# Performance work log

Measured on AMD Instinct MI355X. Metric: run time of the kernel, lower is better.

The kernel has to match this reference:

```python
import jax, jax.numpy as jnp
import numpy as np

HID = 256      # cfg.MODEL.YOSO.HIDDEN_DIM
NPROP = 100    # cfg.MODEL.YOSO.NUM_PROPOSALS
K1 = 3         # CONV_KERNEL_SIZE_1D
K2 = 1         # CONV_KERNEL_SIZE_2D
NCLS = 80      # NUM_CLASSES
NHEAD = 8

def layernorm(x, g, b, eps=1e-5):
    m = jnp.mean(x, -1, keepdims=True)
    v = jnp.var(x, -1, keepdims=True)
    return (x - m) * jax.lax.rsqrt(v + eps) * g + b

def dysep(query, value, Wl, bl, ng, nb):
    # dynamic depthwise conv (kernel K1 along feature axis, one kernel per proposal)
    # followed by dynamic pointwise NxN conv, per torch F.conv1d semantics (cross-correlation, 'same' pad)
    w = query @ Wl + bl                      # [B,N,N+K1]
    dw = w[..., :K1]                         # [B,N,K1] depthwise kernels
    pw = w[..., K1:]                         # [B,N,N]  pointwise mixing
    C = value.shape[-1]
    pad = K1 // 2
    vp = jnp.pad(value, ((0, 0), (0, 0), (pad, pad)))
    depth = sum(dw[..., k:k + 1] * vp[..., k:k + C] for k in range(K1))
    depth = jax.nn.relu(depth)
    point = jnp.einsum('bmn,bnc->bmc', pw, depth)
    return layernorm(point, ng, nb)

def mha(x, in_w, in_b, out_w, out_b):
    B, N, E = x.shape
    d = E // NHEAD
    qkv = x @ in_w + in_b
    q, k, v = jnp.split(qkv, 3, axis=-1)
    q = q.reshape(B, N, NHEAD, d)
    k = k.reshape(B, N, NHEAD, d)
    v = v.reshape(B, N, NHEAD, d)
    att = jnp.einsum('bqhd,bkhd->bhqk', q, k) / jnp.sqrt(jnp.asarray(d, x.dtype))
    att = jax.nn.softmax(att, axis=-1)
    o = jnp.einsum('bhqk,bkhd->bqhd', att, v).reshape(B, N, E)
    return o @ out_w + out_b

def setup_inputs() -> dict:
    key = jax.random.key(0)
    ks = iter(jax.random.split(key, 64))
    B, H, W = 8, 128, 128
    E = HID * K2 * K2
    nrm = lambda *s: jax.random.normal(next(ks), s, jnp.float32) * 0.02
    bias_value = -np.log((1 - 0.01) / 0.01)
    return dict(
        features=jax.random.normal(next(ks), (B, HID, H, W), jnp.float32),
        proposal_kernels=jax.random.normal(next(ks), (B, NPROP, E), jnp.float32),
        mask_preds=jax.random.normal(next(ks), (B, NPROP, H, W), jnp.float32),
        fW=nrm(E, NPROP + K1), fb=jnp.zeros(NPROP + K1), fng=jnp.ones(E), fnb=jnp.zeros(E),
        f_norm_g=jnp.ones(E), f_norm_b=jnp.zeros(E),
        kW=nrm(E, NPROP + K1), kb=jnp.zeros(NPROP + K1), kng=jnp.ones(E), knb=jnp.zeros(E),
        k_norm_g=jnp.ones(E), k_norm_b=jnp.zeros(E),
        attn_in_w=nrm(E, 3 * E), attn_in_b=jnp.zeros(3 * E),
        attn_out_w=nrm(E, E), attn_out_b=jnp.zeros(E),
        s_norm_g=jnp.ones(E), s_norm_b=jnp.zeros(E),
        ffn_w1=nrm(HID, 2048), ffn_b1=jnp.zeros(2048),
        ffn_w2=nrm(2048, HID), ffn_b2=jnp.zeros(HID),
        ffn_norm_g=jnp.ones(HID), ffn_norm_b=jnp.zeros(HID),
        cls_w=nrm(HID, HID), cls_ln_g=jnp.ones(HID), cls_ln_b=jnp.zeros(HID),
        fc_cls_w=nrm(HID, NCLS + 1), fc_cls_b=jnp.full((NCLS + 1,), bias_value, jnp.float32),
        mask_w=nrm(3, HID, HID), mask_ln_g=jnp.ones((3, HID)), mask_ln_b=jnp.zeros((3, HID)),
        fc_mask_w=nrm(HID, HID), fc_mask_b=jnp.zeros(HID),
        train_flag=1,
    )

def reference(features, proposal_kernels, mask_preds, fW, fb, fng, fnb, f_norm_g, f_norm_b,
              kW, kb, kng, knb, k_norm_g, k_norm_b,
              attn_in_w, attn_in_b, attn_out_w, attn_out_b, s_norm_g, s_norm_b,
              ffn_w1, ffn_b1, ffn_w2, ffn_b2, ffn_norm_g, ffn_norm_b,
              cls_w, cls_ln_g, cls_ln_b, fc_cls_w, fc_cls_b,
              mask_w, mask_ln_g, mask_ln_b, fc_mask_w, fc_mask_b, train_flag):
    B, C, H, W = features.shape
    hard = (jax.nn.sigmoid(mask_preds) > 0.5).astype(features.dtype)   # hard masks (no grad path)
    f = jnp.einsum('bnhw,bchw->bnc', hard, features)                   # mask-pooled features [B,N,E]
    k = proposal_kernels.reshape(B, NPROP, -1)
    f = layernorm(f + dysep(k, f, fW, fb, fng, fnb), f_norm_g, f_norm_b)
    kk = layernorm(f + dysep(k, f, kW, kb, kng, knb), k_norm_g, k_norm_b)
    kk = layernorm(kk + mha(kk, attn_in_w, attn_in_b, attn_out_w, attn_out_b), s_norm_g, s_norm_b)
    obj = jnp.transpose(kk.reshape(B, NPROP, HID, -1), (0, 1, 3, 2))   # [B,N,K2*K2,HID]
    h = jax.nn.relu(obj @ ffn_w1 + ffn_b1)
    obj = layernorm(obj + (h @ ffn_w2 + ffn_b2), ffn_norm_g, ffn_norm_b)
    cls_feat = obj.sum(-2)                                             # [B,N,HID]
    mask_feat = obj
    if train_flag:
        cls_feat = jax.nn.relu(layernorm(cls_feat @ cls_w, cls_ln_g, cls_ln_b))
        cls_score = (cls_feat @ fc_cls_w + fc_cls_b).reshape(B, NPROP, -1)
    else:
        cls_score = None
    for i in range(mask_w.shape[0]):
        mask_feat = jax.nn.relu(layernorm(mask_feat @ mask_w[i], mask_ln_g[i], mask_ln_b[i]))
    mask_kernels = (mask_feat @ fc_mask_w + fc_mask_b)[:, :, 0, :]     # squeeze(2), K2*K2==1
    new_mask_preds = jnp.einsum('bqc,bchw->bqhw', mask_kernels, features)
    obj_out = jnp.transpose(obj, (0, 1, 3, 2)).reshape(B, NPROP, HID, K2, K2)
    return (cls_score, new_mask_preds, obj_out)
```

## Files before the change

kernel.cpp:

```cpp
#include <hip/hip_runtime.h>

typedef float f32x4 __attribute__((ext_vector_type(4)));
typedef short bfrag __attribute__((ext_vector_type(8)));
typedef short sh4 __attribute__((ext_vector_type(4)));

__device__ __forceinline__ unsigned short f2bf(float x) {
  unsigned int u = __float_as_uint(x);
  return (unsigned short)((u + 0x7FFFu + ((u >> 16) & 1u)) >> 16);
}
__device__ __forceinline__ float bf2f(unsigned short u) {
  return __uint_as_float(((unsigned int)u) << 16);
}
__device__ __forceinline__ float wred_sum(float v) {
#pragma unroll
  for (int o = 32; o > 0; o >>= 1) v += __shfl_xor(v, o);
  return v;
}
__device__ __forceinline__ float wred_max(float v) {
#pragma unroll
  for (int o = 32; o > 0; o >>= 1) v = fmaxf(v, __shfl_xor(v, o));
  return v;
}

struct Prep6 {
  const float* s[6];
  int K[6];
  int N[6];
  int base[6];
  int doff[6];
};

__global__ __launch_bounds__(256) void prep_w(Prep6 p, unsigned short* wt) {
  int t = blockIdx.x;
  int wi = 0;
#pragma unroll
  for (int i = 0; i < 5; ++i)
    if (t >= p.base[i + 1]) wi = i + 1;
  int lt = t - p.base[wi];
  int K = p.K[wi], N = p.N[wi];
  int tkn = (K + 31) >> 5;
  int tk = lt % tkn, tn = lt / tkn;
  __shared__ float tile[32][33];
  const float* src = p.s[wi];
#pragma unroll
  for (int i = 0; i < 4; ++i) {
    int flat = i * 256 + threadIdx.x;
    int kl = flat >> 5, nl = flat & 31;
    int k = tk * 32 + kl, n = tn * 32 + nl;
    tile[kl][nl] = (k < K && n < N) ? src[(size_t)k * N + n] : 0.f;
  }
  __syncthreads();
  unsigned short* dst = wt + p.doff[wi];
#pragma unroll
  for (int i = 0; i < 4; ++i) {
    int flat = i * 256 + threadIdx.x;
    int nl = flat >> 5, kl = flat & 31;
    int k = tk * 32 + kl, n = tn * 32 + nl;
    if (k < K && n < N) {
      int np = (wi < 2) ? ((n >= 3) ? n - 3 : n + 100) : n;
      dst[(size_t)np * K + k] = f2bf(tile[kl][nl]);
    }
  }
}

__global__ __launch_bounds__(256) void prep_bias(const float* __restrict__ fb_,
                                                 const float* __restrict__ kb_,
                                                 float* __restrict__ bf,
                                                 float* __restrict__ bk) {
  int t = threadIdx.x;
  if (t < 103) {
    int np = (t >= 3) ? t - 3 : t + 100;
    bf[np] = fb_[t];
    bk[np] = kb_[t];
  }
  if (t == 103) { bf[103] = 0.f; bk[103] = 0.f; }
}

struct Cast4 {
  const float* s[4];
  int n[4];
  int base[4];
  int doff[4];
};

__global__ __launch_bounds__(256) void cast_w(Cast4 cc, unsigned short* dst) {
  int t = blockIdx.x;
  int wi = 0;
#pragma unroll
  for (int i = 0; i < 3; ++i)
    if (t >= cc.base[i + 1]) wi = i + 1;
  int lt = t - cc.base[wi];
  int idx = lt * 1024 + threadIdx.x * 4;
  if (idx + 3 < cc.n[wi]) {
    float4 v = *(const float4*)(cc.s[wi] + idx);
    sh4 o;
    o[0] = (short)f2bf(v.x); o[1] = (short)f2bf(v.y);
    o[2] = (short)f2bf(v.z); o[3] = (short)f2bf(v.w);
    *(sh4*)(dst + cc.doff[wi] + idx) = o;
  }
}

__global__ __launch_bounds__(256) void pack_bits(const float* __restrict__ mask,
                                                 unsigned int* __restrict__ bits) {
  int tid = threadIdx.x;
  size_t f = (size_t)blockIdx.x * 256 + tid;
  float4 m = *(const float4*)(mask + f * 4);
  unsigned int n = (m.x > 0.f ? 1u : 0u) | (m.y > 0.f ? 2u : 0u) |
                   (m.z > 0.f ? 4u : 0u) | (m.w > 0.f ? 8u : 0u);
  n <<= ((tid & 7) * 4);
  n |= (unsigned int)__shfl_xor((int)n, 1);
  n |= (unsigned int)__shfl_xor((int)n, 2);
  n |= (unsigned int)__shfl_xor((int)n, 4);
  if ((tid & 7) == 0) bits[((size_t)blockIdx.x * 32) + (tid >> 3)] = n;
}

template <int ABF, int OBF>
__global__ __launch_bounds__(256) void gemm_mf(const void* Av,
                                               const unsigned short* __restrict__ Wt,
                                               const float* __restrict__ bias,
                                               void* Cv, int M, int K, int N, int ldc, int relu) {
  __shared__ short Al[64 * 72];
  __shared__ short Wl[64 * 72];
  int tid = threadIdx.x;
  int r0 = blockIdx.x * 64;
  int c0 = blockIdx.y * 64;
  int w = tid >> 6, lane = tid & 63, quad = lane >> 4, l15 = lane & 15;

  f32x4 acc[4];
#pragma unroll
  for (int mt = 0; mt < 4; ++mt) {
    acc[mt][0] = 0.f; acc[mt][1] = 0.f; acc[mt][2] = 0.f; acc[mt][3] = 0.f;
  }

  for (int k0 = 0; k0 < K; k0 += 64) {
    if (ABF) {
      const unsigned short* A = (const unsigned short*)Av;
#pragma unroll
      for (int p = 0; p < 2; ++p) {
        int flat = p * 256 + tid;
        int row = flat >> 3, k8 = flat & 7;
        bfrag v;
        if (r0 + row < M)
          v = *(const bfrag*)(A + (size_t)(r0 + row) * K + k0 + k8 * 8);
        else
          v = (bfrag)(short)0;
        *(bfrag*)(Al + row * 72 + k8 * 8) = v;
      }
    } else {
      const float* A = (const float*)Av;
#pragma unroll
      for (int p = 0; p < 4; ++p) {
        int flat = p * 256 + tid;
        int row = flat >> 4, c4 = flat & 15;
        sh4 o4;
        if (r0 + row < M) {
          float4 v = *(const float4*)(A + (size_t)(r0 + row) * K + k0 + c4 * 4);
          o4[0] = (short)f2bf(v.x); o4[1] = (short)f2bf(v.y);
          o4[2] = (short)f2bf(v.z); o4[3] = (short)f2bf(v.w);
        } else {
          o4[0] = 0; o4[1] = 0; o4[2] = 0; o4[3] = 0;
        }
        *(sh4*)(Al + row * 72 + c4 * 4) = o4;
      }
    }
#pragma unroll
    for (int p = 0; p < 2; ++p) {
      int flat = p * 256 + tid;
      int row = flat >> 3, k8 = flat & 7;
      bfrag v;
      if (c0 + row < N)
        v = *(const bfrag*)(Wt + (size_t)(c0 + row) * K + k0 + k8 * 8);
      else
        v = (bfrag)(short)0;
      *(bfrag*)(Wl + row * 72 + k8 * 8) = v;
    }
    __syncthreads();
#pragma unroll
    for (int kk = 0; kk < 2; ++kk) {
      bfrag bv = *(const bfrag*)(Wl + (w * 16 + l15) * 72 + kk * 32 + quad * 8);
#pragma unroll
      for (int mt = 0; mt < 4; ++mt) {
        bfrag av = *(const bfrag*)(Al + (mt * 16 + l15) * 72 + kk * 32 + quad * 8);
        acc[mt] = __builtin_amdgcn_mfma_f32_16x16x32_bf16(av, bv, acc[mt], 0, 0, 0);
      }
    }
    __syncthreads();
  }
  int col = c0 + w * 16 + l15;
  if (col < N) {
    float bv = bias ? bias[col] : 0.f;
#pragma unroll
    for (int mt = 0; mt < 4; ++mt)
#pragma unroll
      for (int r = 0; r < 4; ++r) {
        int m = r0 + mt * 16 + quad * 4 + r;
        if (m < M) {
          float v = acc[mt][r] + bv;
          if (relu) v = fmaxf(v, 0.f);
          if (OBF)
            ((unsigned short*)Cv)[(size_t)m * ldc + col] = f2bf(v);
          else
            ((float*)Cv)[(size_t)m * ldc + col] = v;
        }
      }
  }
}

__global__ __launch_bounds__(512, 4) void phaseA(const unsigned int* __restrict__ bits,
                                                 const float* __restrict__ feat,
                                                 float* __restrict__ partial) {
  int tid = threadIdx.x;
  int ks = blockIdx.x;
  int ct = blockIdx.y;
  int b  = blockIdx.z;
  __shared__ short Al[2][112 * 72];
  __shared__ short Bl[2][128 * 72];
  int w = tid >> 6, lane = tid & 63, quad = lane >> 4, l15 = lane & 15;

  int rbase = tid >> 4;
  int c4 = tid & 15;
  const float* frow = feat + (size_t)(b * 256 + ct * 128 + rbase) * 16384 + c4 * 4;

  int arow = tid >> 2, q = tid & 3;
  bool aact = tid < 400;
  const unsigned int* brow = bits + (size_t)(b * 100 + arow) * 512 + (q >> 1);

  f32x4 acc[7];
#pragma unroll
  for (int mt = 0; mt < 7; ++mt) {
    acc[mt][0] = 0.f; acc[mt][1] = 0.f; acc[mt][2] = 0.f; acc[mt][3] = 0.f;
  }

  for (int z = tid; z < 384; z += 512) {
    int bufi = z / 192, rem = z % 192;
    sh4 zz; zz[0] = 0; zz[1] = 0; zz[2] = 0; zz[3] = 0;
    *(sh4*)(&Al[bufi][(100 + (rem >> 4)) * 72 + (rem & 15) * 4]) = zz;
  }

  int k0 = ks * 512;
  {
    float4 bpf[4];
    unsigned int awd = 0;
#pragma unroll
    for (int p = 0; p < 4; ++p)
      bpf[p] = *(const float4*)(frow + (size_t)p * 32 * 16384 + k0);
    if (aact) awd = brow[k0 >> 5];
#pragma unroll
    for (int p = 0; p < 4; ++p) {
      int row = rbase + 32 * p;
      sh4 o4b;
      o4b[0] = (short)f2bf(bpf[p].x);
      o4b[1] = (short)f2bf(bpf[p].y);
      o4b[2] = (short)f2bf(bpf[p].z);
      o4b[3] = (short)f2bf(bpf[p].w);
      *(sh4*)(&Bl[0][row * 72 + c4 * 4]) = o4b;
    }
    if (aact) {
      unsigned int hw16 = (awd >> ((q & 1) * 16)) & 0xFFFFu;
      bfrag e0, e1;
#pragma unroll
      for (int i = 0; i < 8; ++i) e0[i] = ((hw16 >> i) & 1u) ? (short)0x3F80 : (short)0;
#pragma unroll
      for (int i = 0; i < 8; ++i) e1[i] = ((hw16 >> (i + 8)) & 1u) ? (short)0x3F80 : (short)0;
      *(bfrag*)(&Al[0][arow * 72 + q * 16]) = e0;
      *(bfrag*)(&Al[0][arow * 72 + q * 16 + 8]) = e1;
    }
  }
  __syncthreads();

  int cur = 0;
  for (int st = 0; st < 8; ++st) {
    float4 bpf[4];
    unsigned int awd = 0;
    if (st < 7) {
      int kb = k0 + (st + 1) * 64;
#pragma unroll
      for (int p = 0; p < 4; ++p)
        bpf[p] = *(const float4*)(frow + (size_t)p * 32 * 16384 + kb);
      if (aact) awd = brow[kb >> 5];
    }
#pragma unroll
    for (int kk = 0; kk < 2; ++kk) {
      bfrag bv = *(const bfrag*)(&Bl[cur][(w * 16 + l15) * 72 + kk * 32 + quad * 8]);
#pragma unroll
      for (int mt = 0; mt < 7; ++mt) {
        bfrag av = *(const bfrag*)(&Al[cur][(mt * 16 + l15) * 72 + kk * 32 + quad * 8]);
        acc[mt] = __builtin_amdgcn_mfma_f32_16x16x32_bf16(av, bv, acc[mt], 0, 0, 0);
      }
    }
    __builtin_amdgcn_sched_barrier(0);
    if (st < 7) {
      int nxt = cur ^ 1;
#pragma unroll
      for (int p = 0; p < 4; ++p) {
        int row = rbase + 32 * p;
        sh4 o4b;
        o4b[0] = (short)f2bf(bpf[p].x);
        o4b[1] = (short)f2bf(bpf[p].y);
        o4b[2] = (short)f2bf(bpf[p].z);
        o4b[3] = (short)f2bf(bpf[p].w);
        *(sh4*)(&Bl[nxt][row * 72 + c4 * 4]) = o4b;
      }
      if (aact) {
        unsigned int hw16 = (awd >> ((q & 1) * 16)) & 0xFFFFu;
        bfrag e0, e1;
#pragma unroll
        for (int i = 0; i < 8; ++i) e0[i] = ((hw16 >> i) & 1u) ? (short)0x3F80 : (short)0;
#pragma unroll
        for (int i = 0; i < 8; ++i) e1[i] = ((hw16 >> (i + 8)) & 1u) ? (short)0x3F80 : (short)0;
        *(bfrag*)(&Al[nxt][arow * 72 + q * 16]) = e0;
        *(bfrag*)(&Al[nxt][arow * 72 + q * 16 + 8]) = e1;
      }
    }
    __syncthreads();
    cur ^= 1;
  }

  float* pb = partial + (size_t)(b * 32 + ks) * (100 * 256) + ct * 128 + w * 16 + l15;
#pragma unroll
  for (int mt = 0; mt < 7; ++mt)
#pragma unroll
    for (int r = 0; r < 4; ++r) {
      int m = mt * 16 + quad * 4 + r;
      if (m < 100) pb[(size_t)m * 256] = acc[mt][r];
    }
}

__global__ __launch_bounds__(256) void reduceA(const float* __restrict__ partial,
                                               float* __restrict__ fm) {
  int gid = blockIdx.x * 256 + threadIdx.x;
  int c = gid & 255, row = gid >> 8;
  int b = row / 100, n = row % 100;
  float s = 0.f;
#pragma unroll
  for (int ks = 0; ks < 32; ++ks)
    s += partial[((size_t)(b * 32 + ks) * 100 + n) * 256 + c];
  fm[(size_t)row * 256 + c] = s;
}

__global__ __launch_bounds__(256) void pointdw(const float* __restrict__ fm,
                                               const float* __restrict__ wbuf,
                                               float* __restrict__ point) {
  int tid = threadIdx.x;
  int b = blockIdx.y, c0 = blockIdx.x * 32;
  __shared__ float dl[100 * 33];
  for (int flat = tid; flat < 3200; flat += 256) {
    int n = flat >> 5, cl = flat & 31, c = c0 + cl;
    const float* fr = fm + (size_t)(b * 100 + n) * 256;
    const float* wr = wbuf + (size_t)(b * 100 + n) * 104;
    float x0 = (c > 0) ? fr[c - 1] : 0.f;
    float x1 = fr[c];
    float x2 = (c < 255) ? fr[c + 1] : 0.f;
    float d = wr[100] * x0 + wr[101] * x1 + wr[102] * x2;
    dl[n * 33 + cl] = fmaxf(d, 0.f);
  }
  __syncthreads();
  int cl = tid & 31, mg = tid >> 5;
  for (int m = mg; m < 100; m += 8) {
    const float4* pw4 = (const float4*)(wbuf + (size_t)(b * 100 + m) * 104);
    float a = 0.f;
#pragma unroll
    for (int n4 = 0; n4 < 25; ++n4) {
      float4 wv = pw4[n4];
      a += wv.x * dl[(n4 * 4 + 0) * 33 + cl] + wv.y * dl[(n4 * 4 + 1) * 33 + cl]
         + wv.z * dl[(n4 * 4 + 2) * 33 + cl] + wv.w * dl[(n4 * 4 + 3) * 33 + cl];
    }
    point[(size_t)(b * 100 + m) * 256 + c0 + cl] = a;
  }
}

__global__ __launch_bounds__(256) void ln2_kernel(const float* __restrict__ x,
                                                  const float* __restrict__ resid,
                                                  const float* __restrict__ g1, const float* __restrict__ b1,
                                                  const float* __restrict__ g2, const float* __restrict__ b2,
                                                  float* __restrict__ out) {
  int tid = threadIdx.x;
  int row = blockIdx.x * 4 + (tid >> 6);
  int lane = tid & 63;
  size_t base = (size_t)row * 256 + lane * 4;
  float4 v = *(const float4*)(x + base);
  float mean = wred_sum(v.x + v.y + v.z + v.w) * (1.f / 256.f);
  float d0 = v.x - mean, d1 = v.y - mean, d2 = v.z - mean, d3 = v.w - mean;
  float rs = rsqrtf(wred_sum(d0 * d0 + d1 * d1 + d2 * d2 + d3 * d3) * (1.f / 256.f) + 1e-5f);
  float4 gv = *(const float4*)(g1 + lane * 4);
  float4 bv = *(const float4*)(b1 + lane * 4);
  float4 rv = *(const float4*)(resid + base);
  float y0 = rv.x + d0 * rs * gv.x + bv.x;
  float y1 = rv.y + d1 * rs * gv.y + bv.y;
  float y2 = rv.z + d2 * rs * gv.z + bv.z;
  float y3 = rv.w + d3 * rs * gv.w + bv.w;
  float mean2 = wred_sum(y0 + y1 + y2 + y3) * (1.f / 256.f);
  float e0 = y0 - mean2, e1 = y1 - mean2, e2 = y2 - mean2, e3 = y3 - mean2;
  float rs2 = rsqrtf(wred_sum(e0 * e0 + e1 * e1 + e2 * e2 + e3 * e3) * (1.f / 256.f) + 1e-5f);
  float4 g2v = *(const float4*)(g2 + lane * 4);
  float4 b2v = *(const float4*)(b2 + lane * 4);
  float4 o;
  o.x = e0 * rs2 * g2v.x + b2v.x;
  o.y = e1 * rs2 * g2v.y + b2v.y;
  o.z = e2 * rs2 * g2v.z + b2v.z;
  o.w = e3 * rs2 * g2v.w + b2v.w;
  *(float4*)(out + base) = o;
}

__global__ __launch_bounds__(256) void ln_kernel(const float* __restrict__ x,
                                                 const float* __restrict__ res,
                                                 const float* __restrict__ g, const float* __restrict__ bb,
                                                 float* __restrict__ out, int relu,
                                                 float* __restrict__ copy2) {
  int tid = threadIdx.x;
  int row = blockIdx.x * 4 + (tid >> 6);
  int lane = tid & 63;
  size_t base = (size_t)row * 256 + lane * 4;
  float4 v = *(const float4*)(x + base);
  if (res) {
    float4 rv = *(const float4*)(res + base);
    v.x += rv.x; v.y += rv.y; v.z += rv.z; v.w += rv.w;
  }
  float mean = wred_sum(v.x + v.y + v.z + v.w) * (1.f / 256.f);
  float d0 = v.x - mean, d1 = v.y - mean, d2 = v.z - mean, d3 = v.w - mean;
  float rs = rsqrtf(wred_sum(d0 * d0 + d1 * d1 + d2 * d2 + d3 * d3) * (1.f / 256.f) + 1e-5f);
  float4 gv = *(const float4*)(g + lane * 4);
  float4 bv = *(const float4*)(bb + lane * 4);
  float4 o;
  o.x = d0 * rs * gv.x + bv.x;
  o.y = d1 * rs * gv.y + bv.y;
  o.z = d2 * rs * gv.z + bv.z;
  o.w = d3 * rs * gv.w + bv.w;
  if (relu) {
    o.x = fmaxf(o.x, 0.f); o.y = fmaxf(o.y, 0.f);
    o.z = fmaxf(o.z, 0.f); o.w = fmaxf(o.w, 0.f);
  }
  *(float4*)(out + base) = o;
  if (copy2) *(float4*)(copy2 + base) = o;
}

__global__ __launch_bounds__(256) void attn_kernel(const float* __restrict__ qkv,
                                                   float* __restrict__ obuf) {
  int tid = threadIdx.x;
  int b = blockIdx.y, h = blockIdx.x;
  __shared__ float ktj[100 * 32];
  __shared__ unsigned short vl[100 * 32];
  __shared__ float sl[100 * 100];
  const float* base = qkv + (size_t)b * 100 * 768;
  for (int flat = tid; flat < 3200; flat += 256) {
    int j = flat >> 5, dd = flat & 31;
    ktj[j * 32 + dd] = base[(size_t)j * 768 + 256 + h * 32 + dd];
    vl[j * 32 + dd] = f2bf(base[(size_t)j * 768 + 512 + h * 32 + dd]);
  }
  __syncthreads();
  {
    int i = tid >> 1;
    int jh = (tid & 1) * 50;
    int qi = (i < 100) ? i : 0;
    const float4* q4 = (const float4*)(base + (size_t)qi * 768 + h * 32);
    float4 q[8];
#pragma unroll
    for (int d4 = 0; d4 < 8; ++d4) q[d4] = q4[d4];
    if (i < 100) {
      for (int jj = 0; jj < 50; ++jj) {
        int j = jh + jj;
        const float4* kr = (const float4*)(ktj + j * 32);
        float a = 0.f;
#pragma unroll
        for (int d4 = 0; d4 < 8; ++d4) {
          float4 kv = kr[d4];
          a += q[d4].x * kv.x + q[d4].y * kv.y + q[d4].z * kv.z + q[d4].w * kv.w;
        }
        sl[i * 100 + j] = a * 0.17677669529663687f;
      }
    }
  }
  __syncthreads();
  int w = tid >> 6, lane = tid & 63;
  for (int r = w; r < 100; r += 4) {
    float x0 = sl[r * 100 + lane];
    float x1 = (lane + 64 < 100) ? sl[r * 100 + lane + 64] : -1e30f;
    float mx = wred_max(fmaxf(x0, x1));
    float e0 = __expf(x0 - mx);
    float e1 = (lane + 64 < 100) ? __expf(x1 - mx) : 0.f;
    float inv = 1.f / wred_sum(e0 + e1);
    sl[r * 100 + lane] = e0 * inv;
    if (lane + 64 < 100) sl[r * 100 + lane + 64] = e1 * inv;
  }
  __syncthreads();
  for (int flat = tid; flat < 3200; flat += 256) {
    int i = flat >> 5, dd = flat & 31;
    float a = 0.f;
#pragma unroll 4
    for (int j = 0; j < 100; ++j) a += sl[i * 100 + j] * bf2f(vl[j * 32 + dd]);
    obuf[(size_t)(b * 100 + i) * 256 + h * 32 + dd] = a;
  }
}

__global__ __launch_bounds__(256) void head_fused(
    const float* __restrict__ objb,
    const unsigned short* __restrict__ whd,
    const float* __restrict__ cls_g, const float* __restrict__ cls_b,
    const float* __restrict__ fcclsb,
    const float* __restrict__ mask_g, const float* __restrict__ mask_b,
    const float* __restrict__ fcmb,
    float* __restrict__ out_cls, unsigned short* __restrict__ mk16) {
  const int WH_CLS = 0, WH_FCCLS = 65536, WH_M = 86272, WH_FCM = 282880;
  int tid = threadIdx.x, wv = tid >> 6, lane = tid & 63;
  int row = blockIdx.x;
  __shared__ float xs[256];
  __shared__ float x0s[256];
  __shared__ float ps[4][256];
  if (wv == 0) {
    float4 v = *(const float4*)(objb + (size_t)row * 256 + lane * 4);
    *(float4*)(&xs[lane * 4]) = v;
    *(float4*)(&x0s[lane * 4]) = v;
  }
  __syncthreads();
  int c = lane * 4;
  int kb = wv * 64;

  for (int li = 0; li < 3; ++li) {
    const unsigned short* W = whd + WH_M + li * 65536;
    float a0 = 0.f, a1 = 0.f, a2 = 0.f, a3 = 0.f;
#pragma unroll 8
    for (int k = kb; k < kb + 64; ++k) {
      float xk = xs[k];
      sh4 w4 = *(const sh4*)(W + (size_t)k * 256 + c);
      a0 += xk * bf2f((unsigned short)w4[0]);
      a1 += xk * bf2f((unsigned short)w4[1]);
      a2 += xk * bf2f((unsigned short)w4[2]);
      a3 += xk * bf2f((unsigned short)w4[3]);
    }
    ps[wv][c] = a0; ps[wv][c + 1] = a1; ps[wv][c + 2] = a2; ps[wv][c + 3] = a3;
    __syncthreads();
    float s0 = ps[0][c] + ps[1][c] + ps[2][c] + ps[3][c];
    float s1 = ps[0][c + 1] + ps[1][c + 1] + ps[2][c + 1] + ps[3][c + 1];
    float s2 = ps[0][c + 2] + ps[1][c + 2] + ps[2][c + 2] + ps[3][c + 2];
    float s3 = ps[0][c + 3] + ps[1][c + 3] + ps[2][c + 3] + ps[3][c + 3];
    float mean = wred_sum(s0 + s1 + s2 + s3) * (1.f / 256.f);
    float d0 = s0 - mean, d1 = s1 - mean, d2 = s2 - mean, d3 = s3 - mean;
    float rs = rsqrtf(wred_sum(d0 * d0 + d1 * d1 + d2 * d2 + d3 * d3) * (1.f / 256.f) + 1e-5f);
    float4 gv = *(const float4*)(mask_g + li * 256 + c);
    float4 bv = *(const float4*)(mask_b + li * 256 + c);
    float4 o;
    o.x = fmaxf(d0 * rs * gv.x + bv.x, 0.f);
    o.y = fmaxf(d1 * rs * gv.y + bv.y, 0.f);
    o.z = fmaxf(d2 * rs * gv.z + bv.z, 0.f);
    o.w = fmaxf(d3 * rs * gv.w + bv.w, 0.f);
    __syncthreads();
    *(float4*)(&xs[c]) = o;
    __syncthreads();
  }
  {
    const unsigned short* W = whd + WH_FCM;
    float a0 = 0.f, a1 = 0.f, a2 = 0.f, a3 = 0.f;
#pragma unroll 8
    for (int k = kb; k < kb + 64; ++k) {
      float xk = xs[k];
      sh4 w4 = *(const sh4*)(W + (size_t)k * 256 + c);
      a0 += xk * bf2f((unsigned short)w4[0]);
      a1 += xk * bf2f((unsigned short)w4[1]);
      a2 += xk * bf2f((unsigned short)w4[2]);
      a3 += xk * bf2f((unsigned short)w4[3]);
    }
    ps[wv][c] = a0; ps[wv][c + 1] = a1; ps[wv][c + 2] = a2; ps[wv][c + 3] = a3;
    __syncthreads();
    if (wv == 0) {
      float s0 = ps[0][c] + ps[1][c] + ps[2][c] + ps[3][c];
      float s1 = ps[0][c + 1] + ps[1][c + 1] + ps[2][c + 1] + ps[3][c + 1];
      float s2 = ps[0][c + 2] + ps[1][c + 2] + ps[2][c + 2] + ps[3][c + 2];
      float s3 = ps[0][c + 3] + ps[1][c + 3] + ps[2][c + 3] + ps[3][c + 3];
      float4 bv = *(const float4*)(fcmb + c);
      sh4 o;
      o[0] = (short)f2bf(s0 + bv.x); o[1] = (short)f2bf(s1 + bv.y);
      o[2] = (short)f2bf(s2 + bv.z); o[3] = (short)f2bf(s3 + bv.w);
      *(sh4*)(mk16 + (size_t)row * 256 + c) = o;
    }
    __syncthreads();
  }
  {
    const unsigned short* W = whd + WH_CLS;
    float a0 = 0.f, a1 = 0.f, a2 = 0.f, a3 = 0.f;
#pragma unroll 8
    for (int k = kb; k < kb + 64; ++k) {
      float xk = x0s[k];
      sh4 w4 = *(const sh4*)(W + (size_t)k * 256 + c);
      a0 += xk * bf2f((unsigned short)w4[0]);
      a1 += xk * bf2f((unsigned short)w4[1]);
      a2 += xk * bf2f((unsigned short)w4[2]);
      a3 += xk * bf2f((unsigned short)w4[3]);
    }
    ps[wv][c] = a0; ps[wv][c + 1] = a1; ps[wv][c + 2] = a2; ps[wv][c + 3] = a3;
    __syncthreads();
    float s0 = ps[0][c] + ps[1][c] + ps[2][c] + ps[3][c];
    float s1 = ps[0][c + 1] + ps[1][c + 1] + ps[2][c + 1] + ps[3][c + 1];
    float s2 = ps[0][c + 2] + ps[1][c + 2] + ps[2][c + 2] + ps[3][c + 2];
    float s3 = ps[0][c + 3] + ps[1][c + 3] + ps[2][c + 3] + ps[3][c + 3];
    float mean = wred_sum(s0 + s1 + s2 + s3) * (1.f / 256.f);
    float d0 = s0 - mean, d1 = s1 - mean, d2 = s2 - mean, d3 = s3 - mean;
    float rs = rsqrtf(wred_sum(d0 * d0 + d1 * d1 + d2 * d2 + d3 * d3) * (1.f / 256.f) + 1e-5f);
    float4 gv = *(const float4*)(cls_g + c);
    float4 bv = *(const float4*)(cls_b + c);
    float4 o;
    o.x = fmaxf(d0 * rs * gv.x + bv.x, 0.f);
    o.y = fmaxf(d1 * rs * gv.y + bv.y, 0.f);
    o.z = fmaxf(d2 * rs * gv.z + bv.z, 0.f);
    o.w = fmaxf(d3 * rs * gv.w + bv.w, 0.f);
    __syncthreads();
    *(float4*)(&xs[c]) = o;
    __syncthreads();
  }
  {
    const unsigned short* W = whd + WH_FCCLS;
    float a0 = 0.f, a1 = 0.f;
#pragma unroll 8
    for (int k = kb; k < kb + 64; ++k) {
      float xk = xs[k];
      a0 += xk * bf2f(W[(size_t)k * 81 + lane]);
      if (lane < 17) a1 += xk * bf2f(W[(size_t)k * 81 + 64 + lane]);
    }
    ps[wv][lane] = a0;
    if (lane < 17) ps[wv][64 + lane] = a1;
    __syncthreads();
    if (wv == 0) {
      float s = ps[0][lane] + ps[1][lane] + ps[2][lane] + ps[3][lane];
      out_cls[(size_t)row * 81 + lane] = s + fcclsb[lane];
      if (lane < 17) {
        float s2 = ps[0][64 + lane] + ps[1][64 + lane] + ps[2][64 + lane] + ps[3][64 + lane];
        out_cls[(size_t)row * 81 + 64 + lane] = s2 + fcclsb[64 + lane];
      }
    }
  }
}

__global__ __launch_bounds__(256, 4) void phaseE(const unsigned short* __restrict__ mk16,
                                                 const float* __restrict__ feat,
                                                 float* __restrict__ out) {
  int tid = threadIdx.x;
  int b = blockIdx.y;
  int hw0 = blockIdx.x * 128;
  int w = tid >> 6, lane = tid & 63, quad = lane >> 4, l15 = lane & 15;
  f32x4 acc[7][2];
#pragma unroll
  for (int mt = 0; mt < 7; ++mt)
#pragma unroll
    for (int nt = 0; nt < 2; ++nt) {
      acc[mt][nt][0] = 0.f; acc[mt][nt][1] = 0.f; acc[mt][nt][2] = 0.f; acc[mt][nt][3] = 0.f;
    }
  size_t fb = (size_t)b * 256 * 16384;
  int hwl = hw0 + w * 32 + l15;
  const unsigned short* mkb_b = mk16 + (size_t)b * 100 * 256;
  for (int kk = 0; kk < 8; ++kk) {
    bfrag bv[2];
#pragma unroll
    for (int nt = 0; nt < 2; ++nt) {
#pragma unroll
      for (int j = 0; j < 8; ++j) {
        float v = feat[fb + (size_t)(kk * 32 + quad * 8 + j) * 16384 + hwl + nt * 16];
        bv[nt][j] = (short)f2bf(v);
      }
    }
    bfrag av[7];
#pragma unroll
    for (int mt = 0; mt < 7; ++mt) {
      int row = mt * 16 + l15;
      int rr = (row < 100) ? row : 0;
      av[mt] = *(const bfrag*)(mkb_b + (size_t)rr * 256 + kk * 32 + quad * 8);
    }
#pragma unroll
    for (int mt = 0; mt < 7; ++mt) {
      acc[mt][0] = __builtin_amdgcn_mfma_f32_16x16x32_bf16(av[mt], bv[0], acc[mt][0], 0, 0, 0);
      acc[mt][1] = __builtin_amdgcn_mfma_f32_16x16x32_bf16(av[mt], bv[1], acc[mt][1], 0, 0, 0);
    }
  }
#pragma unroll
  for (int mt = 0; mt < 7; ++mt)
#pragma unroll
    for (int nt = 0; nt < 2; ++nt)
#pragma unroll
      for (int r = 0; r < 4; ++r) {
        int m = mt * 16 + quad * 4 + r;
        if (m < 100)
          out[(size_t)(b * 100 + m) * 16384 + hw0 + w * 32 + nt * 16 + l15] = acc[mt][nt][r];
      }
}

extern "C" void kernel_launch(void* const* d_in, const int* in_sizes, int n_in,
                              void* d_out, int out_size, void* d_ws, size_t ws_size,
                              hipStream_t stream) {
  const float* feat    = (const float*)d_in[0];
  const float* prop    = (const float*)d_in[1];
  const float* maskp   = (const float*)d_in[2];
  const float* fW      = (const float*)d_in[3];
  const float* fb_     = (const float*)d_in[4];
  const float* fng     = (const float*)d_in[5];
  const float* fnb     = (const float*)d_in[6];
  const float* f_ng    = (const float*)d_in[7];
  const float* f_nb    = (const float*)d_in[8];
  const float* kW      = (const float*)d_in[9];
  const float* kb_     = (const float*)d_in[10];
  const float* kng     = (const float*)d_in[11];
  const float* knb     = (const float*)d_in[12];
  const float* k_ng    = (const float*)d_in[13];
  const float* k_nb    = (const float*)d_in[14];
  const float* aw_in   = (const float*)d_in[15];
  const float* ab_in   = (const float*)d_in[16];
  const float* aw_out  = (const float*)d_in[17];
  const float* ab_out  = (const float*)d_in[18];
  const float* s_ng    = (const float*)d_in[19];
  const float* s_nb    = (const float*)d_in[20];
  const float* w1      = (const float*)d_in[21];
  const float* b1      = (const float*)d_in[22];
  const float* w2      = (const float*)d_in[23];
  const float* b2      = (const float*)d_in[24];
  const float* ffn_ng  = (const float*)d_in[25];
  const float* ffn_nb  = (const float*)d_in[26];
  const float* cls_w   = (const float*)d_in[27];
  const float* cls_g   = (const float*)d_in[28];
  const float* cls_b   = (const float*)d_in[29];
  const float* fcclsw  = (const float*)d_in[30];
  const float* fcclsb  = (const float*)d_in[31];
  const float* mask_w  = (const float*)d_in[32];
  const float* mask_g  = (const float*)d_in[33];
  const float* mask_b  = (const float*)d_in[34];
  const float* fcmw    = (const float*)d_in[35];
  const float* fcmb    = (const float*)d_in[36];
  float* out = (float*)d_out;

  float* ws = (float*)d_ws;
  size_t off = 0;
  unsigned short* wt = (unsigned short*)(ws + off); off += 681984;
  float* fm     = ws + off; off += 204800;
  float* bias_f = ws + off; off += 104;
  float* bias_k = ws + off; off += 104;
  unsigned int* bitsbuf = (unsigned int*)(ws + off); off += 409600;
  unsigned short* whd = (unsigned short*)(ws + off); off += 174208;
  float* partial = ws + off;
  float* ub = partial;
  size_t uo = 0;
  float* wb   = ub + uo; uo += 83200;
  float* pt   = ub + uo; uo += 204800;
  float* fbuf = ub + uo; uo += 204800;
  float* kkb  = ub + uo; uo += 204800;
  float* qkvb = ub + uo; uo += 614400;
  float* ob   = ub + uo; uo += 204800;
  float* mo   = ub + uo; uo += 204800;
  float* kk2  = ub + uo; uo += 204800;
  float* t1   = ub + uo; uo += 204800;
  float* objb = ub + uo; uo += 204800;
  float* mkb  = ub + uo; uo += 204800;
  unsigned short* ffn1b = (unsigned short*)(ub + uo); uo += 409600;
  unsigned short* mkb16 = (unsigned short*)mkb;

  const int wt_fW = 0, wt_kW = 26624, wt_ain = 53248, wt_aout = 249856;
  const int wt_w1 = 315392, wt_w2 = 839680;

  float* out_cls  = out;
  float* out_mask = out + 64800;
  float* out_obj  = out + 64800 + 13107200;

  Prep6 p;
  const float* srcs[6] = {fW, kW, aw_in, aw_out, w1, w2};
  int Ks[6]    = {256, 256, 256, 256, 256, 2048};
  int Ns[6]    = {103, 103, 768, 256, 2048, 256};
  int doffs[6] = {wt_fW, wt_kW, wt_ain, wt_aout, wt_w1, wt_w2};
  int tb = 0;
  for (int i = 0; i < 6; ++i) {
    p.s[i] = srcs[i]; p.K[i] = Ks[i]; p.N[i] = Ns[i]; p.doff[i] = doffs[i];
    p.base[i] = tb;
    tb += ((Ks[i] + 31) / 32) * ((Ns[i] + 31) / 32);
  }
  prep_w<<<tb, 256, 0, stream>>>(p, wt);
  prep_bias<<<1, 256, 0, stream>>>(fb_, kb_, bias_f, bias_k);
  Cast4 cc;
  const float* csrc[4] = {cls_w, fcclsw, mask_w, fcmw};
  int cn[4] = {65536, 20736, 196608, 65536};
  int cdoff[4] = {0, 65536, 86272, 282880};
  int cb = 0;
  for (int i = 0; i < 4; ++i) {
    cc.s[i] = csrc[i]; cc.n[i] = cn[i]; cc.doff[i] = cdoff[i];
    cc.base[i] = cb;
    cb += (cn[i] + 1023) / 1024;
  }
  cast_w<<<cb, 256, 0, stream>>>(cc, whd);
  pack_bits<<<12800, 256, 0, stream>>>(maskp, bitsbuf);

  phaseA<<<dim3(32, 2, 8), 512, 0, stream>>>(bitsbuf, feat, partial);
  reduceA<<<800, 256, 0, stream>>>(partial, fm);
  gemm_mf<0, 0><<<dim3(13, 2), 256, 0, stream>>>(prop, wt + wt_fW, bias_f, wb, 800, 256, 103, 104, 0);
  pointdw<<<dim3(8, 8), 256, 0, stream>>>(fm, wb, pt);
  ln2_kernel<<<200, 256, 0, stream>>>(pt, fm, fng, fnb, f_ng, f_nb, fbuf);
  gemm_mf<0, 0><<<dim3(13, 2), 256, 0, stream>>>(prop, wt + wt_kW, bias_k, wb, 800, 256, 103, 104, 0);
  pointdw<<<dim3(8, 8), 256, 0, stream>>>(fbuf, wb, pt);
  ln2_kernel<<<200, 256, 0, stream>>>(pt, fbuf, kng, knb, k_ng, k_nb, kkb);
  gemm_mf<0, 0><<<dim3(13, 12), 256, 0, stream>>>(kkb, wt + wt_ain, ab_in, qkvb, 800, 256, 768, 768, 0);
  attn_kernel<<<dim3(8, 8), 256, 0, stream>>>(qkvb, ob);
  gemm_mf<0, 0><<<dim3(13, 4), 256, 0, stream>>>(ob, wt + wt_aout, ab_out, mo, 800, 256, 256, 256, 0);
  ln_kernel<<<200, 256, 0, stream>>>(mo, kkb, s_ng, s_nb, kk2, 0, nullptr);
  gemm_mf<0, 1><<<dim3(13, 32), 256, 0, stream>>>(kk2, wt + wt_w1, b1, ffn1b, 800, 256, 2048, 2048, 1);
  gemm_mf<1, 0><<<dim3(13, 4), 256, 0, stream>>>(ffn1b, wt + wt_w2, b2, t1, 800, 2048, 256, 256, 0);
  ln_kernel<<<200, 256, 0, stream>>>(t1, kk2, ffn_ng, ffn_nb, objb, 0, out_obj);
  head_fused<<<800, 256, 0, stream>>>(objb, whd, cls_g, cls_b, fcclsb,
                                      mask_g, mask_b, fcmb, out_cls, mkb16);
  phaseE<<<dim3(128, 8), 256, 0, stream>>>(mkb16, feat, out_mask);
}
```

Measured before the change: 655.9 us.

## Merge dysep weight GEMMs, split-K the FFN2 GEMM, and split attention queries

```diff
diff --git a/kernel.cpp b/kernel.cpp
--- a/kernel.cpp
+++ b/kernel.cpp
@@ -65,15 +65,14 @@
 
 __global__ __launch_bounds__(256) void prep_bias(const float* __restrict__ fb_,
                                                  const float* __restrict__ kb_,
-                                                 float* __restrict__ bf,
-                                                 float* __restrict__ bk) {
+                                                 float* __restrict__ bfk) {
   int t = threadIdx.x;
   if (t < 103) {
     int np = (t >= 3) ? t - 3 : t + 100;
-    bf[np] = fb_[t];
-    bk[np] = kb_[t];
-  }
-  if (t == 103) { bf[103] = 0.f; bk[103] = 0.f; }
+    bfk[np] = fb_[t];
+    bfk[104 + np] = kb_[t];
+  }
+  if (t == 103) { bfk[103] = 0.f; bfk[207] = 0.f; }
 }
 
 struct Cast4 {
@@ -118,12 +117,14 @@
 __global__ __launch_bounds__(256) void gemm_mf(const void* Av,
                                                const unsigned short* __restrict__ Wt,
                                                const float* __restrict__ bias,
-                                               void* Cv, int M, int K, int N, int ldc, int relu) {
+                                               void* Cv, int M, int K, int N, int ldc, int relu,
+                                               int kspan) {
   __shared__ short Al[64 * 72];
   __shared__ short Wl[64 * 72];
   int tid = threadIdx.x;
   int r0 = blockIdx.x * 64;
   int c0 = blockIdx.y * 64;
+  int kz = blockIdx.z * kspan;
   int w = tid >> 6, lane = tid & 63, quad = lane >> 4, l15 = lane & 15;
 
   f32x4 acc[4];
@@ -132,7 +133,7 @@
     acc[mt][0] = 0.f; acc[mt][1] = 0.f; acc[mt][2] = 0.f; acc[mt][3] = 0.f;
   }
 
-  for (int k0 = 0; k0 < K; k0 += 64) {
+  for (int k0 = kz; k0 < kz + kspan; k0 += 64) {
     if (ABF) {
       const unsigned short* A = (const unsigned short*)Av;
 #pragma unroll
@@ -189,6 +190,7 @@
   int col = c0 + w * 16 + l15;
   if (col < N) {
     float bv = bias ? bias[col] : 0.f;
+    size_t zoff = (size_t)blockIdx.z * M * ldc;
 #pragma unroll
     for (int mt = 0; mt < 4; ++mt)
 #pragma unroll
@@ -198,9 +200,9 @@
           float v = acc[mt][r] + bv;
           if (relu) v = fmaxf(v, 0.f);
           if (OBF)
-            ((unsigned short*)Cv)[(size_t)m * ldc + col] = f2bf(v);
+            ((unsigned short*)Cv)[zoff + (size_t)m * ldc + col] = f2bf(v);
           else
-            ((float*)Cv)[(size_t)m * ldc + col] = v;
+            ((float*)Cv)[zoff + (size_t)m * ldc + col] = v;
         }
       }
   }
@@ -347,7 +349,7 @@
   for (int flat = tid; flat < 3200; flat += 256) {
     int n = flat >> 5, cl = flat & 31, c = c0 + cl;
     const float* fr = fm + (size_t)(b * 100 + n) * 256;
-    const float* wr = wbuf + (size_t)(b * 100 + n) * 104;
+    const float* wr = wbuf + (size_t)(b * 100 + n) * 208;
     float x0 = (c > 0) ? fr[c - 1] : 0.f;
     float x1 = fr[c];
     float x2 = (c < 255) ? fr[c + 1] : 0.f;
@@ -357,7 +359,7 @@
   __syncthreads();
   int cl = tid & 31, mg = tid >> 5;
   for (int m = mg; m < 100; m += 8) {
-    const float4* pw4 = (const float4*)(wbuf + (size_t)(b * 100 + m) * 104);
+    const float4* pw4 = (const float4*)(wbuf + (size_t)(b * 100 + m) * 208);
     float a = 0.f;
 #pragma unroll
     for (int n4 = 0; n4 < 25; ++n4) {
@@ -434,13 +436,46 @@
   if (copy2) *(float4*)(copy2 + base) = o;
 }
 
+__global__ __launch_bounds__(256) void ln_ffn2(const float* __restrict__ t1,
+                                               const float* __restrict__ b2,
+                                               const float* __restrict__ res,
+                                               const float* __restrict__ g, const float* __restrict__ bb,
+                                               float* __restrict__ out,
+                                               float* __restrict__ copy2) {
+  int tid = threadIdx.x;
+  int row = blockIdx.x * 4 + (tid >> 6);
+  int lane = tid & 63;
+  size_t base = (size_t)row * 256 + lane * 4;
+  float4 v = *(const float4*)(t1 + base);
+#pragma unroll
+  for (int s = 1; s < 4; ++s) {
+    float4 p = *(const float4*)(t1 + (size_t)s * 204800 + base);
+    v.x += p.x; v.y += p.y; v.z += p.z; v.w += p.w;
+  }
+  float4 b2v = *(const float4*)(b2 + lane * 4);
+  float4 rv = *(const float4*)(res + base);
+  v.x += b2v.x + rv.x; v.y += b2v.y + rv.y; v.z += b2v.z + rv.z; v.w += b2v.w + rv.w;
+  float mean = wred_sum(v.x + v.y + v.z + v.w) * (1.f / 256.f);
+  float d0 = v.x - mean, d1 = v.y - mean, d2 = v.z - mean, d3 = v.w - mean;
+  float rs = rsqrtf(wred_sum(d0 * d0 + d1 * d1 + d2 * d2 + d3 * d3) * (1.f / 256.f) + 1e-5f);
+  float4 gv = *(const float4*)(g + lane * 4);
+  float4 bv = *(const float4*)(bb + lane * 4);
+  float4 o;
+  o.x = d0 * rs * gv.x + bv.x;
+  o.y = d1 * rs * gv.y + bv.y;
+  o.z = d2 * rs * gv.z + bv.z;
+  o.w = d3 * rs * gv.w + bv.w;
+  *(float4*)(out + base) = o;
+  *(float4*)(copy2 + base) = o;
+}
+
 __global__ __launch_bounds__(256) void attn_kernel(const float* __restrict__ qkv,
                                                    float* __restrict__ obuf) {
   int tid = threadIdx.x;
-  int b = blockIdx.y, h = blockIdx.x;
+  int b = blockIdx.y, h = blockIdx.x & 7, qq = blockIdx.x >> 3;
   __shared__ float ktj[100 * 32];
   __shared__ unsigned short vl[100 * 32];
-  __shared__ float sl[100 * 100];
+  __shared__ float sl[25 * 100];
   const float* base = qkv + (size_t)b * 100 * 768;
   for (int flat = tid; flat < 3200; flat += 256) {
     int j = flat >> 5, dd = flat & 31;
@@ -449,16 +484,16 @@
   }
   __syncthreads();
   {
-    int i = tid >> 1;
-    int jh = (tid & 1) * 50;
-    int qi = (i < 100) ? i : 0;
-    const float4* q4 = (const float4*)(base + (size_t)qi * 768 + h * 32);
+    int il = tid % 25;
+    int jseg = tid / 25;
+    int i = qq * 25 + il;
+    const float4* q4 = (const float4*)(base + (size_t)i * 768 + h * 32);
     float4 q[8];
 #pragma unroll
     for (int d4 = 0; d4 < 8; ++d4) q[d4] = q4[d4];
-    if (i < 100) {
-      for (int jj = 0; jj < 50; ++jj) {
-        int j = jh + jj;
+    if (jseg < 10) {
+      for (int jj = 0; jj < 10; ++jj) {
+        int j = jseg * 10 + jj;
         const float4* kr = (const float4*)(ktj + j * 32);
         float a = 0.f;
 #pragma unroll
@@ -466,13 +501,13 @@
           float4 kv = kr[d4];
           a += q[d4].x * kv.x + q[d4].y * kv.y + q[d4].z * kv.z + q[d4].w * kv.w;
         }
-        sl[i * 100 + j] = a * 0.17677669529663687f;
+        sl[il * 100 + j] = a * 0.17677669529663687f;
       }
     }
   }
   __syncthreads();
   int w = tid >> 6, lane = tid & 63;
-  for (int r = w; r < 100; r += 4) {
+  for (int r = w; r < 25; r += 4) {
     float x0 = sl[r * 100 + lane];
     float x1 = (lane + 64 < 100) ? sl[r * 100 + lane + 64] : -1e30f;
     float mx = wred_max(fmaxf(x0, x1));
@@ -483,12 +518,12 @@
     if (lane + 64 < 100) sl[r * 100 + lane + 64] = e1 * inv;
   }
   __syncthreads();
-  for (int flat = tid; flat < 3200; flat += 256) {
-    int i = flat >> 5, dd = flat & 31;
+  for (int flat = tid; flat < 800; flat += 256) {
+    int il = flat >> 5, dd = flat & 31;
     float a = 0.f;
 #pragma unroll 4
-    for (int j = 0; j < 100; ++j) a += sl[i * 100 + j] * bf2f(vl[j * 32 + dd]);
-    obuf[(size_t)(b * 100 + i) * 256 + h * 32 + dd] = a;
+    for (int j = 0; j < 100; ++j) a += sl[il * 100 + j] * bf2f(vl[j * 32 + dd]);
+    obuf[(size_t)(b * 100 + qq * 25 + il) * 256 + h * 32 + dd] = a;
   }
 }
 
@@ -726,15 +761,14 @@
   float* ws = (float*)d_ws;
   size_t off = 0;
   unsigned short* wt = (unsigned short*)(ws + off); off += 681984;
-  float* fm     = ws + off; off += 204800;
-  float* bias_f = ws + off; off += 104;
-  float* bias_k = ws + off; off += 104;
+  float* fm      = ws + off; off += 204800;
+  float* bias_fk = ws + off; off += 208;
   unsigned int* bitsbuf = (unsigned int*)(ws + off); off += 409600;
   unsigned short* whd = (unsigned short*)(ws + off); off += 174208;
   float* partial = ws + off;
   float* ub = partial;
   size_t uo = 0;
-  float* wb   = ub + uo; uo += 83200;
+  float* wb   = ub + uo; uo += 166400;
   float* pt   = ub + uo; uo += 204800;
   float* fbuf = ub + uo; uo += 204800;
   float* kkb  = ub + uo; uo += 204800;
@@ -742,7 +776,7 @@
   float* ob   = ub + uo; uo += 204800;
   float* mo   = ub + uo; uo += 204800;
   float* kk2  = ub + uo; uo += 204800;
-  float* t1   = ub + uo; uo += 204800;
+  float* t1   = ub + uo; uo += 819200;
   float* objb = ub + uo; uo += 204800;
   float* mkb  = ub + uo; uo += 204800;
   unsigned short* ffn1b = (unsigned short*)(ub + uo); uo += 409600;
@@ -767,7 +801,7 @@
     tb += ((Ks[i] + 31) / 32) * ((Ns[i] + 31) / 32);
   }
   prep_w<<<tb, 256, 0, stream>>>(p, wt);
-  prep_bias<<<1, 256, 0, stream>>>(fb_, kb_, bias_f, bias_k);
+  prep_bias<<<1, 256, 0, stream>>>(fb_, kb_, bias_fk);
   Cast4 cc;
   const float* csrc[4] = {cls_w, fcclsw, mask_w, fcmw};
   int cn[4] = {65536, 20736, 196608, 65536};
@@ -783,19 +817,18 @@
 
   phaseA<<<dim3(32, 2, 8), 512, 0, stream>>>(bitsbuf, feat, partial);
   reduceA<<<800, 256, 0, stream>>>(partial, fm);
-  gemm_mf<0, 0><<<dim3(13, 2), 256, 0, stream>>>(prop, wt + wt_fW, bias_f, wb, 800, 256, 103, 104, 0);
+  gemm_mf<0, 0><<<dim3(13, 4, 1), 256, 0, stream>>>(prop, wt + wt_fW, bias_fk, wb, 800, 256, 208, 208, 0, 256);
   pointdw<<<dim3(8, 8), 256, 0, stream>>>(fm, wb, pt);
   ln2_kernel<<<200, 256, 0, stream>>>(pt, fm, fng, fnb, f_ng, f_nb, fbuf);
-  gemm_mf<0, 0><<<dim3(13, 2), 256, 0, stream>>>(prop, wt + wt_kW, bias_k, wb, 800, 256, 103, 104, 0);
-  pointdw<<<dim3(8, 8), 256, 0, stream>>>(fbuf, wb, pt);
+  pointdw<<<dim3(8, 8), 256, 0, stream>>>(fbuf, wb + 104, pt);
   ln2_kernel<<<200, 256, 0, stream>>>(pt, fbuf, kng, knb, k_ng, k_nb, kkb);
-  gemm_mf<0, 0><<<dim3(13, 12), 256, 0, stream>>>(kkb, wt + wt_ain, ab_in, qkvb, 800, 256, 768, 768, 0);
-  attn_kernel<<<dim3(8, 8), 256, 0, stream>>>(qkvb, ob);
-  gemm_mf<0, 0><<<dim3(13, 4), 256, 0, stream>>>(ob, wt + wt_aout, ab_out, mo, 800, 256, 256, 256, 0);
+  gemm_mf<0, 0><<<dim3(13, 12, 1), 256, 0, stream>>>(kkb, wt + wt_ain, ab_in, qkvb, 800, 256, 768, 768, 0, 256);
+  attn_kernel<<<dim3(32, 8), 256, 0, stream>>>(qkvb, ob);
+  gemm_mf<0, 0><<<dim3(13, 4, 1), 256, 0, stream>>>(ob, wt + wt_aout, ab_out, mo, 800, 256, 256, 256, 0, 256);
   ln_kernel<<<200, 256, 0, stream>>>(mo, kkb, s_ng, s_nb, kk2, 0, nullptr);
-  gemm_mf<0, 1><<<dim3(13, 32), 256, 0, stream>>>(kk2, wt + wt_w1, b1, ffn1b, 800, 256, 2048, 2048, 1);
-  gemm_mf<1, 0><<<dim3(13, 4), 256, 0, stream>>>(ffn1b, wt + wt_w2, b2, t1, 800, 2048, 256, 256, 0);
-  ln_kernel<<<200, 256, 0, stream>>>(t1, kk2, ffn_ng, ffn_nb, objb, 0, out_obj);
+  gemm_mf<0, 1><<<dim3(13, 32, 1), 256, 0, stream>>>(kk2, wt + wt_w1, b1, ffn1b, 800, 256, 2048, 2048, 1, 256);
+  gemm_mf<1, 0><<<dim3(13, 4, 4), 256, 0, stream>>>(ffn1b, wt + wt_w2, nullptr, t1, 800, 2048, 256, 256, 0, 512);
+  ln_ffn2<<<200, 256, 0, stream>>>(t1, b2, kk2, ffn_ng, ffn_nb, objb, out_obj);
   head_fused<<<800, 256, 0, stream>>>(objb, whd, cls_g, cls_b, fcclsb,
                                       mask_g, mask_b, fcmb, out_cls, mkb16);
   phaseE<<<dim3(128, 8), 256, 0, stream>>>(mkb16, feat, out_mask);
```

Result: faster. 588.0 us (-10.3%).
